# Kernel tuning notes

Measured on AMD Instinct MI355X. Metric: run time of the kernel, lower is better.

Reference implementation:

```python
import jax, jax.numpy as jnp
import numpy as np


def setup_inputs() -> dict:
    key = jax.random.key(0)
    ks = jax.random.split(key, 6)
    T, B, D, H = 512, 64, 512, 512
    s = 1.0 / np.sqrt(H)  # PyTorch-style uniform-ish scale kept simple as scaled normal
    return {
        "inputs": jax.random.normal(ks[0], (T, B, D), jnp.float32),
        "mask": jnp.ones((T, B), jnp.float32),
        "h0": jax.random.normal(ks[1], (B, H), jnp.float32),
        "W_ih": jax.random.normal(ks[2], (4 * H, D), jnp.float32) * s,
        "W_hh": jax.random.normal(ks[3], (4 * H, H), jnp.float32) * s,
        "b_ih": jax.random.normal(ks[4], (4 * H,), jnp.float32) * s,
        "b_hh": jax.random.normal(ks[5], (4 * H,), jnp.float32) * s,
    }


def _lstm_forward(inputs, mask, h0, c0, W_ih, W_hh, b_ih, b_hh):
    """Masked LSTM over time. inputs [T,B,D], mask [T,B], h0/c0 [B,H].
    Mask blend resets state toward the initial hidden where mask==0,
    exactly as the torch loop does per step."""
    bias = b_ih + b_hh
    # Precompute input projections for all steps: [T,B,4H]
    x_proj = jnp.einsum("tbd,gd->tbg", inputs, W_ih) + bias

    def step(carry, inp):
        h, c = carry
        xg, mt = inp  # xg [B,4H], mt [B]
        gates = xg + h @ W_hh.T
        i, f, g, o = jnp.split(gates, 4, axis=-1)
        i = jax.nn.sigmoid(i)
        f = jax.nn.sigmoid(f)
        g = jnp.tanh(g)
        o = jax.nn.sigmoid(o)
        c_new = f * c + i * g
        h_new = o * jnp.tanh(c_new)
        m = mt[:, None]
        h_new = h_new * m + h0 * (1.0 - m)
        c_new = c_new * m + c0 * (1.0 - m)
        return (h_new, c_new), h_new

    (hT, cT), outs = jax.lax.scan(step, (h0, c0), (x_proj, mask))
    return outs, hT, cT


def reference(inputs, mask, h0, W_ih, W_hh, b_ih, b_hh):
    # torch module uses the SAME random tensor for h0 and c0
    out, hT, cT = _lstm_forward(inputs, mask, h0, h0, W_ih, W_hh, b_ih, b_hh)
    # hidden = (stack over layers) -> [1,B,H] each for single layer
    return out, hT[None], cT[None]
```

## Files before the change

### kernel.cpp

```cpp
#include <hip/hip_runtime.h>
#include <hip/hip_fp16.h>


#define T_DIM 512
#define B_DIM 64
#define D_DIM 512
#define H_DIM 512
#define M_DIM (T_DIM * B_DIM)

#define NGROUP 8
#define BPG 32
#define NBLK (NGROUP * BPG)
#define NTHR 512
#define WS 520

typedef __attribute__((ext_vector_type(8))) _Float16 half8;
typedef __attribute__((ext_vector_type(2))) __fp16 fp16x2;
typedef __attribute__((ext_vector_type(4))) float float4v;

#define AT_LD_I(p)    __hip_atomic_load((p), __ATOMIC_RELAXED, __HIP_MEMORY_SCOPE_AGENT)
#define AT_ST_I(p, v) __hip_atomic_store((p), (v), __ATOMIC_RELAXED, __HIP_MEMORY_SCOPE_AGENT)
#define AT_LD64(p)    __hip_atomic_load((p), __ATOMIC_RELAXED, __HIP_MEMORY_SCOPE_AGENT)
#define AT_ST64(p, v) __hip_atomic_store((p), (v), __ATOMIC_RELAXED, __HIP_MEMORY_SCOPE_AGENT)

__device__ __forceinline__ float sigf(float x) { return 1.0f / (1.0f + __expf(-x)); }
__device__ __forceinline__ float tanhfast(float x) { return 2.0f / (1.0f + __expf(-2.0f * x)) - 1.0f; }
__device__ __forceinline__ unsigned short f2h(float x) {
  return __builtin_bit_cast(unsigned short, (_Float16)x);
}
__device__ __forceinline__ unsigned pk2h(float a, float b) {
  fp16x2 h = __builtin_amdgcn_cvt_pkrtz(a, b);
  return __builtin_bit_cast(unsigned, h);
}

__global__ __launch_bounds__(NTHR) void lstm_seq(
    const float* __restrict__ inputs, const float* __restrict__ mask,
    const float* __restrict__ h0, const float* __restrict__ Whh,
    const float* __restrict__ Wih, const float* __restrict__ b_ih,
    const float* __restrict__ b_hh,
    float* __restrict__ out, unsigned short* __restrict__ hbuf,
    int* slot_base) {
  extern __shared__ char smemc[];
  unsigned short* Wl = (unsigned short*)smemc;
  unsigned short* Xw = Wl + 64 * WS;
  unsigned short* hl = Xw + 64 * WS;
  float* part = (float*)(hl + 16 * WS);

  const int tid = threadIdx.x;
  const int blk = blockIdx.x;
  const int grp = blk & 7;
  const int rank = blk >> 3;
  const int bbase = grp * 8;
  const int jbase = rank * 16;
  int* slots = (int*)((char*)slot_base + grp * 128);

  for (int idx = tid; idx < 64 * 128; idx += NTHR) {
    int r = idx >> 7;
    int k4 = (idx & 127) << 2;
    int grow = (r >> 4) * H_DIM + jbase + (r & 15);
    float4 wv = *(const float4*)(Whh + (size_t)grow * H_DIM + k4);
    *(uint2*)(Wl + r * WS + k4) = make_uint2(pk2h(wv.x, wv.y), pk2h(wv.z, wv.w));
    float4 xv = *(const float4*)(Wih + (size_t)grow * D_DIM + k4);
    *(uint2*)(Xw + r * WS + k4) = make_uint2(pk2h(xv.x, xv.y), pk2h(xv.z, xv.w));
  }

  const int eb = tid >> 4, ejl = tid & 15;
  const int bglob = bbase + eb;
  const int jglob = jbase + ejl;
  float h0v = 0.0f, cval = 0.0f, mval = 1.f;
  float bi_ = 0.f, bf_ = 0.f, bg_ = 0.f, bo_ = 0.f;
  if (tid < 128) {
    h0v = h0[bglob * H_DIM + jglob];
    cval = h0v;
    bi_ = b_ih[0 * H_DIM + jglob] + b_hh[0 * H_DIM + jglob];
    bf_ = b_ih[1 * H_DIM + jglob] + b_hh[1 * H_DIM + jglob];
    bg_ = b_ih[2 * H_DIM + jglob] + b_hh[2 * H_DIM + jglob];
    bo_ = b_ih[3 * H_DIM + jglob] + b_hh[3 * H_DIM + jglob];
  }

  {
    int mybits = (tid < 128) ? (int)f2h(h0v) : 0;
    int nb1 = __shfl_down(mybits, 1, 64);
    int nb2 = __shfl_down(mybits, 2, 64);
    int nb3 = __shfl_down(mybits, 3, 64);
    if (tid < 128 && ((ejl & 3) == 0)) {
      unsigned lo = (unsigned)mybits | ((unsigned)nb1 << 16);
      unsigned hi = (unsigned)nb2 | ((unsigned)nb3 << 16);
      AT_ST64((unsigned long long*)hbuf + bglob * 128 + (jglob >> 2),
              ((unsigned long long)hi << 32) | lo);
    }
  }
  __syncthreads();
  if (tid == 0) AT_ST_I(&slots[rank], 1);
  if (tid < 128) mval = mask[bglob];

  const int w = tid >> 6;
  const int lane = tid & 63;
  const int q = w & 3;
  const int ks = w >> 2;
  const int am = lane & 15;
  const int koct = (lane >> 4) * 8;
  const int br = q * 16 + (lane & 15);

  float4v xacc = {0.f, 0.f, 0.f, 0.f};
  {
    const float* xin = inputs + (size_t)bbase * D_DIM;
#pragma unroll
    for (int i = 0; i < 4; ++i) {
      int idx = tid + i * NTHR;
      int r = idx >> 8;
      int cl = idx & 255;
      float2 xv = *(const float2*)(xin + (size_t)r * D_DIM + cl * 2);
      ((unsigned*)hl)[r * (WS / 2) + cl] = pk2h(xv.x, xv.y);
    }
    __syncthreads();
#pragma unroll
    for (int kc = 0; kc < 8; ++kc) {
      int k = ks * 256 + kc * 32 + koct;
      half8 a = *(const half8*)((const _Float16*)hl + am * WS + k);
      half8 b8 = *(const half8*)((const _Float16*)Xw + br * WS + k);
      xacc = __builtin_amdgcn_mfma_f32_16x16x32_f16(a, b8, xacc, 0, 0, 0);
    }
  }
  if (tid < 64) {
    int v;
    do {
      v = (tid < BPG) ? AT_LD_I(&slots[tid]) : 1;
      if (__all(v >= 1)) break;
      __builtin_amdgcn_s_sleep(2);
    } while (true);
  }
  __syncthreads();
  __asm__ volatile("" ::: "memory");

  for (int ts = 0; ts < T_DIM; ++ts) {
    const unsigned long long* cur64 =
        (const unsigned long long*)hbuf + (ts & 1) * (B_DIM * H_DIM / 4) +
        (size_t)bbase * 128;
    unsigned long long* nxt64 =
        (unsigned long long*)hbuf + ((ts + 1) & 1) * (B_DIM * H_DIM / 4);

#pragma unroll
    for (int i = 0; i < 2; ++i) {
      int v = tid + i * NTHR;
      unsigned long long u = AT_LD64(cur64 + v);
      ((unsigned long long*)hl)[(v >> 7) * 130 + (v & 127)] = u;
    }
    __syncthreads();

    float4v acc = xacc;
#pragma unroll
    for (int kc = 0; kc < 8; ++kc) {
      int k = ks * 256 + kc * 32 + koct;
      half8 a = *(const half8*)((const _Float16*)hl + am * WS + k);
      half8 b8 = *(const half8*)((const _Float16*)Wl + br * WS + k);
      acc = __builtin_amdgcn_mfma_f32_16x16x32_f16(a, b8, acc, 0, 0, 0);
    }
#pragma unroll
    for (int reg = 0; reg < 4; ++reg) {
      int m = (lane >> 4) * 4 + reg;
      part[w * 256 + m * 16 + (lane & 15)] = acc[reg];
    }
    __syncthreads();

    float hnew = 0.f;
    if (tid < 128) {
      int o = eb * 16 + ejl;
      float iv = sigf(part[0 * 256 + o] + part[4 * 256 + o] + bi_);
      float fv = sigf(part[1 * 256 + o] + part[5 * 256 + o] + bf_);
      float gv = tanhfast(part[2 * 256 + o] + part[6 * 256 + o] + bg_);
      float ov = sigf(part[3 * 256 + o] + part[7 * 256 + o] + bo_);
      float cn = fv * cval + iv * gv;
      float hn = ov * tanhfast(cn);
      hnew = hn * mval + h0v * (1.0f - mval);
      cval = cn * mval + h0v * (1.0f - mval);
    }
    {
      int mybits = (tid < 128) ? (int)f2h(hnew) : 0;
      int nb1 = __shfl_down(mybits, 1, 64);
      int nb2 = __shfl_down(mybits, 2, 64);
      int nb3 = __shfl_down(mybits, 3, 64);
      if (tid < 128 && ((ejl & 3) == 0)) {
        unsigned lo = (unsigned)mybits | ((unsigned)nb1 << 16);
        unsigned hi = (unsigned)nb2 | ((unsigned)nb3 << 16);
        AT_ST64(nxt64 + bglob * 128 + (jglob >> 2),
                ((unsigned long long)hi << 32) | lo);
      }
    }
    __syncthreads();
    if (tid == 0) AT_ST_I(&slots[rank], ts + 2);

    if (ts + 1 < T_DIM) {
      const float* xin = inputs + ((size_t)(ts + 1) * B_DIM + bbase) * D_DIM;
#pragma unroll
      for (int i = 0; i < 4; ++i) {
        int idx = tid + i * NTHR;
        int r = idx >> 8;
        int cl = idx & 255;
        float2 xv = *(const float2*)(xin + (size_t)r * D_DIM + cl * 2);
        ((unsigned*)hl)[r * (WS / 2) + cl] = pk2h(xv.x, xv.y);
      }
      __syncthreads();
      if (tid < 128) {
        out[((size_t)ts * B_DIM + bglob) * H_DIM + jglob] = hnew;
        mval = mask[(ts + 1) * B_DIM + bglob];
      }
      float4v xa = {0.f, 0.f, 0.f, 0.f};
#pragma unroll
      for (int kc = 0; kc < 8; ++kc) {
        int k = ks * 256 + kc * 32 + koct;
        half8 a = *(const half8*)((const _Float16*)hl + am * WS + k);
        half8 b8 = *(const half8*)((const _Float16*)Xw + br * WS + k);
        xa = __builtin_amdgcn_mfma_f32_16x16x32_f16(a, b8, xa, 0, 0, 0);
      }
      xacc = xa;
    } else if (tid < 128) {
      out[((size_t)ts * B_DIM + bglob) * H_DIM + jglob] = hnew;
      out[(size_t)T_DIM * B_DIM * H_DIM + bglob * H_DIM + jglob] = hnew;
      out[(size_t)T_DIM * B_DIM * H_DIM + B_DIM * H_DIM + bglob * H_DIM + jglob] = cval;
    }

    if (tid < 64) {
      int v;
      do {
        v = (tid < BPG) ? AT_LD_I(&slots[tid]) : (ts + 2);
        if (__all(v >= ts + 2)) break;
        __builtin_amdgcn_s_sleep(2);
      } while (true);
    }
    __syncthreads();
    __asm__ volatile("" ::: "memory");
  }
}

extern "C" void kernel_launch(void* const* d_in, const int* in_sizes, int n_in,
                              void* d_out, int out_size, void* d_ws, size_t ws_size,
                              hipStream_t stream) {
  const float* inputs = (const float*)d_in[0];
  const float* maskp  = (const float*)d_in[1];
  const float* h0     = (const float*)d_in[2];
  const float* W_ih   = (const float*)d_in[3];
  const float* W_hh   = (const float*)d_in[4];
  const float* b_ih   = (const float*)d_in[5];
  const float* b_hh   = (const float*)d_in[6];
  float* out = (float*)d_out;

  char* ws = (char*)d_ws;
  int* slot_base = (int*)ws;
  unsigned short* hbuf = (unsigned short*)(ws + 4096);

  (void)hipMemsetAsync(d_ws, 0, 4096, stream);

  size_t ldsB = (size_t)(64 * WS * 2 * 2 + 16 * WS * 2 + 2048 * 4);

  lstm_seq<<<NBLK, NTHR, ldsB, stream>>>(inputs, maskp, h0, W_hh, W_ih, b_ih, b_hh,
                                         out, hbuf, slot_base);

  (void)in_sizes; (void)n_in; (void)out_size; (void)ws_size;
}
```

Measured before the change: 1.658 ms.

## Interleave two independent batch groups per block to hide cross-block sync latency

Halves the grid to 128 blocks, each owning two batch groups (A and B) that are stepped alternately, so while one group waits on its peer-barrier the other's work can proceed and the spin wait moves to just before consuming h. The input projection is now computed in the same loop as the recurrent MFMA (two accumulators), with next-step inputs prefetched into registers and stored to separate LDS buffers after the step. MFMA A-operand rows are duplicated (am = lane&7) since only 8 batch rows exist, and only half the lanes write partials. This adds serial work per block and doubles per-block step count, trading parallelism for latency hiding.

```diff
diff --git a/kernel.cpp b/kernel.cpp
--- a/kernel.cpp
+++ b/kernel.cpp
@@ -6,11 +6,9 @@
 #define B_DIM 64
 #define D_DIM 512
 #define H_DIM 512
-#define M_DIM (T_DIM * B_DIM)
-
-#define NGROUP 8
+
 #define BPG 32
-#define NBLK (NGROUP * BPG)
+#define NBLK 128
 #define NTHR 512
 #define WS 520
 
@@ -33,6 +31,20 @@
   return __builtin_bit_cast(unsigned, h);
 }
 
+#define SPIN(slots, tgt)                                          \
+  do {                                                            \
+    if (tid < 64) {                                               \
+      int v_;                                                     \
+      do {                                                        \
+        v_ = (tid < BPG) ? AT_LD_I(&(slots)[tid]) : (tgt);        \
+        if (__all(v_ >= (tgt))) break;                            \
+        __builtin_amdgcn_s_sleep(1);                              \
+      } while (true);                                             \
+    }                                                             \
+    __syncthreads();                                              \
+    __asm__ volatile("" ::: "memory");                            \
+  } while (0)
+
 __global__ __launch_bounds__(NTHR) void lstm_seq(
     const float* __restrict__ inputs, const float* __restrict__ mask,
     const float* __restrict__ h0, const float* __restrict__ Whh,
@@ -41,18 +53,22 @@
     float* __restrict__ out, unsigned short* __restrict__ hbuf,
     int* slot_base) {
   extern __shared__ char smemc[];
-  unsigned short* Wl = (unsigned short*)smemc;
-  unsigned short* Xw = Wl + 64 * WS;
-  unsigned short* hl = Xw + 64 * WS;
-  float* part = (float*)(hl + 16 * WS);
+  unsigned short* Wl  = (unsigned short*)smemc;
+  unsigned short* Xw  = Wl + 64 * WS;
+  unsigned short* hl  = Xw + 64 * WS;
+  unsigned short* xsA = hl + 8 * WS;
+  unsigned short* xsB = xsA + 8 * WS;
+  float* part = (float*)(xsB + 8 * WS);
 
   const int tid = threadIdx.x;
   const int blk = blockIdx.x;
-  const int grp = blk & 7;
-  const int rank = blk >> 3;
-  const int bbase = grp * 8;
+  const int gA = blk & 3;
+  const int rank = blk >> 2;
+  const int bbA = gA * 8;
+  const int bbB = bbA + 32;
   const int jbase = rank * 16;
-  int* slots = (int*)((char*)slot_base + grp * 128);
+  int* slotsA = (int*)((char*)slot_base + gA * 128);
+  int* slotsB = (int*)((char*)slot_base + (gA + 4) * 128);
 
   for (int idx = tid; idx < 64 * 128; idx += NTHR) {
     int r = idx >> 7;
@@ -65,171 +81,233 @@
   }
 
   const int eb = tid >> 4, ejl = tid & 15;
-  const int bglob = bbase + eb;
+  const int bglobA = bbA + eb;
+  const int bglobB = bbB + eb;
   const int jglob = jbase + ejl;
-  float h0v = 0.0f, cval = 0.0f, mval = 1.f;
+  float h0vA = 0.f, cvalA = 0.f, mvalA = 1.f;
+  float h0vB = 0.f, cvalB = 0.f, mvalB = 1.f;
   float bi_ = 0.f, bf_ = 0.f, bg_ = 0.f, bo_ = 0.f;
   if (tid < 128) {
-    h0v = h0[bglob * H_DIM + jglob];
-    cval = h0v;
+    h0vA = h0[bglobA * H_DIM + jglob];  cvalA = h0vA;
+    h0vB = h0[bglobB * H_DIM + jglob];  cvalB = h0vB;
     bi_ = b_ih[0 * H_DIM + jglob] + b_hh[0 * H_DIM + jglob];
     bf_ = b_ih[1 * H_DIM + jglob] + b_hh[1 * H_DIM + jglob];
     bg_ = b_ih[2 * H_DIM + jglob] + b_hh[2 * H_DIM + jglob];
     bo_ = b_ih[3 * H_DIM + jglob] + b_hh[3 * H_DIM + jglob];
-  }
+    mvalA = mask[bglobA];
+    mvalB = mask[bglobB];
+  }
+
+  const int xr0r = tid >> 8,           xc = tid & 255;
+  const int xr1r = (tid + 512) >> 8;
+  const int xr2r = (tid + 1024) >> 8;
+  const int xr3r = (tid + 1536) >> 8;
 
   {
-    int mybits = (tid < 128) ? (int)f2h(h0v) : 0;
-    int nb1 = __shfl_down(mybits, 1, 64);
-    int nb2 = __shfl_down(mybits, 2, 64);
-    int nb3 = __shfl_down(mybits, 3, 64);
+    int mbA = (tid < 128) ? (int)f2h(h0vA) : 0;
+    int mbB = (tid < 128) ? (int)f2h(h0vB) : 0;
+    int a1 = __shfl_down(mbA, 1, 64), a2 = __shfl_down(mbA, 2, 64), a3 = __shfl_down(mbA, 3, 64);
+    int b1 = __shfl_down(mbB, 1, 64), b2 = __shfl_down(mbB, 2, 64), b3 = __shfl_down(mbB, 3, 64);
     if (tid < 128 && ((ejl & 3) == 0)) {
-      unsigned lo = (unsigned)mybits | ((unsigned)nb1 << 16);
-      unsigned hi = (unsigned)nb2 | ((unsigned)nb3 << 16);
-      AT_ST64((unsigned long long*)hbuf + bglob * 128 + (jglob >> 2),
-              ((unsigned long long)hi << 32) | lo);
+      unsigned long long uA = ((unsigned long long)(((unsigned)a2) | ((unsigned)a3 << 16)) << 32) |
+                              (((unsigned)mbA) | ((unsigned)a1 << 16));
+      unsigned long long uB = ((unsigned long long)(((unsigned)b2) | ((unsigned)b3 << 16)) << 32) |
+                              (((unsigned)mbB) | ((unsigned)b1 << 16));
+      AT_ST64((unsigned long long*)hbuf + bglobA * 128 + (jglob >> 2), uA);
+      AT_ST64((unsigned long long*)hbuf + bglobB * 128 + (jglob >> 2), uB);
     }
   }
   __syncthreads();
-  if (tid == 0) AT_ST_I(&slots[rank], 1);
-  if (tid < 128) mval = mask[bglob];
+  if (tid == 0) { AT_ST_I(&slotsA[rank], 1); AT_ST_I(&slotsB[rank], 1); }
+
+  {
+    const float* xa = inputs + (size_t)bbA * D_DIM;
+    const float* xb = inputs + (size_t)bbB * D_DIM;
+    float2 t0 = *(const float2*)(xa + (size_t)xr0r * D_DIM + xc * 2);
+    float2 t1 = *(const float2*)(xa + (size_t)xr1r * D_DIM + xc * 2);
+    float2 t2 = *(const float2*)(xa + (size_t)xr2r * D_DIM + xc * 2);
+    float2 t3 = *(const float2*)(xa + (size_t)xr3r * D_DIM + xc * 2);
+    float2 s0 = *(const float2*)(xb + (size_t)xr0r * D_DIM + xc * 2);
+    float2 s1 = *(const float2*)(xb + (size_t)xr1r * D_DIM + xc * 2);
+    float2 s2 = *(const float2*)(xb + (size_t)xr2r * D_DIM + xc * 2);
+    float2 s3 = *(const float2*)(xb + (size_t)xr3r * D_DIM + xc * 2);
+    ((unsigned*)xsA)[xr0r * (WS / 2) + xc] = pk2h(t0.x, t0.y);
+    ((unsigned*)xsA)[xr1r * (WS / 2) + xc] = pk2h(t1.x, t1.y);
+    ((unsigned*)xsA)[xr2r * (WS / 2) + xc] = pk2h(t2.x, t2.y);
+    ((unsigned*)xsA)[xr3r * (WS / 2) + xc] = pk2h(t3.x, t3.y);
+    ((unsigned*)xsB)[xr0r * (WS / 2) + xc] = pk2h(s0.x, s0.y);
+    ((unsigned*)xsB)[xr1r * (WS / 2) + xc] = pk2h(s1.x, s1.y);
+    ((unsigned*)xsB)[xr2r * (WS / 2) + xc] = pk2h(s2.x, s2.y);
+    ((unsigned*)xsB)[xr3r * (WS / 2) + xc] = pk2h(s3.x, s3.y);
+  }
 
   const int w = tid >> 6;
   const int lane = tid & 63;
-  const int q = w & 3;
   const int ks = w >> 2;
-  const int am = lane & 15;
+  const int am = lane & 7;
   const int koct = (lane >> 4) * 8;
-  const int br = q * 16 + (lane & 15);
-
-  float4v xacc = {0.f, 0.f, 0.f, 0.f};
-  {
-    const float* xin = inputs + (size_t)bbase * D_DIM;
-#pragma unroll
-    for (int i = 0; i < 4; ++i) {
-      int idx = tid + i * NTHR;
-      int r = idx >> 8;
-      int cl = idx & 255;
-      float2 xv = *(const float2*)(xin + (size_t)r * D_DIM + cl * 2);
-      ((unsigned*)hl)[r * (WS / 2) + cl] = pk2h(xv.x, xv.y);
-    }
-    __syncthreads();
-#pragma unroll
-    for (int kc = 0; kc < 8; ++kc) {
-      int k = ks * 256 + kc * 32 + koct;
-      half8 a = *(const half8*)((const _Float16*)hl + am * WS + k);
-      half8 b8 = *(const half8*)((const _Float16*)Xw + br * WS + k);
-      xacc = __builtin_amdgcn_mfma_f32_16x16x32_f16(a, b8, xacc, 0, 0, 0);
-    }
-  }
-  if (tid < 64) {
-    int v;
-    do {
-      v = (tid < BPG) ? AT_LD_I(&slots[tid]) : 1;
-      if (__all(v >= 1)) break;
-      __builtin_amdgcn_s_sleep(2);
-    } while (true);
-  }
-  __syncthreads();
-  __asm__ volatile("" ::: "memory");
+  const int br = (w & 3) * 16 + (lane & 15);
 
   for (int ts = 0; ts < T_DIM; ++ts) {
-    const unsigned long long* cur64 =
-        (const unsigned long long*)hbuf + (ts & 1) * (B_DIM * H_DIM / 4) +
-        (size_t)bbase * 128;
-    unsigned long long* nxt64 =
-        (unsigned long long*)hbuf + ((ts + 1) & 1) * (B_DIM * H_DIM / 4);
-
-#pragma unroll
-    for (int i = 0; i < 2; ++i) {
-      int v = tid + i * NTHR;
-      unsigned long long u = AT_LD64(cur64 + v);
-      ((unsigned long long*)hl)[(v >> 7) * 130 + (v & 127)] = u;
-    }
-    __syncthreads();
-
-    float4v acc = xacc;
-#pragma unroll
-    for (int kc = 0; kc < 8; ++kc) {
-      int k = ks * 256 + kc * 32 + koct;
-      half8 a = *(const half8*)((const _Float16*)hl + am * WS + k);
-      half8 b8 = *(const half8*)((const _Float16*)Wl + br * WS + k);
-      acc = __builtin_amdgcn_mfma_f32_16x16x32_f16(a, b8, acc, 0, 0, 0);
-    }
-#pragma unroll
-    for (int reg = 0; reg < 4; ++reg) {
-      int m = (lane >> 4) * 4 + reg;
-      part[w * 256 + m * 16 + (lane & 15)] = acc[reg];
-    }
-    __syncthreads();
-
-    float hnew = 0.f;
-    if (tid < 128) {
-      int o = eb * 16 + ejl;
-      float iv = sigf(part[0 * 256 + o] + part[4 * 256 + o] + bi_);
-      float fv = sigf(part[1 * 256 + o] + part[5 * 256 + o] + bf_);
-      float gv = tanhfast(part[2 * 256 + o] + part[6 * 256 + o] + bg_);
-      float ov = sigf(part[3 * 256 + o] + part[7 * 256 + o] + bo_);
-      float cn = fv * cval + iv * gv;
-      float hn = ov * tanhfast(cn);
-      hnew = hn * mval + h0v * (1.0f - mval);
-      cval = cn * mval + h0v * (1.0f - mval);
-    }
+    const int xts = (ts + 1 < T_DIM) ? ts + 1 : ts;
+
     {
-      int mybits = (tid < 128) ? (int)f2h(hnew) : 0;
-      int nb1 = __shfl_down(mybits, 1, 64);
-      int nb2 = __shfl_down(mybits, 2, 64);
-      int nb3 = __shfl_down(mybits, 3, 64);
-      if (tid < 128 && ((ejl & 3) == 0)) {
-        unsigned lo = (unsigned)mybits | ((unsigned)nb1 << 16);
-        unsigned hi = (unsigned)nb2 | ((unsigned)nb3 << 16);
-        AT_ST64(nxt64 + bglob * 128 + (jglob >> 2),
-                ((unsigned long long)hi << 32) | lo);
-      }
-    }
-    __syncthreads();
-    if (tid == 0) AT_ST_I(&slots[rank], ts + 2);
-
-    if (ts + 1 < T_DIM) {
-      const float* xin = inputs + ((size_t)(ts + 1) * B_DIM + bbase) * D_DIM;
-#pragma unroll
-      for (int i = 0; i < 4; ++i) {
-        int idx = tid + i * NTHR;
-        int r = idx >> 8;
-        int cl = idx & 255;
-        float2 xv = *(const float2*)(xin + (size_t)r * D_DIM + cl * 2);
-        ((unsigned*)hl)[r * (WS / 2) + cl] = pk2h(xv.x, xv.y);
-      }
-      __syncthreads();
-      if (tid < 128) {
-        out[((size_t)ts * B_DIM + bglob) * H_DIM + jglob] = hnew;
-        mval = mask[(ts + 1) * B_DIM + bglob];
-      }
-      float4v xa = {0.f, 0.f, 0.f, 0.f};
+      const unsigned long long* cur =
+          (const unsigned long long*)hbuf + (ts & 1) * (B_DIM * H_DIM / 4) + (size_t)bbA * 128;
+      unsigned long long* nxt =
+          (unsigned long long*)hbuf + ((ts + 1) & 1) * (B_DIM * H_DIM / 4);
+
+      SPIN(slotsA, ts + 1);
+
+      unsigned long long hld0 = AT_LD64(cur + tid);
+      unsigned long long hld1 = AT_LD64(cur + tid + NTHR);
+      const float* xin = inputs + ((size_t)xts * B_DIM + bbA) * D_DIM;
+      float2 a0 = *(const float2*)(xin + (size_t)xr0r * D_DIM + xc * 2);
+      float2 a1 = *(const float2*)(xin + (size_t)xr1r * D_DIM + xc * 2);
+      float2 a2 = *(const float2*)(xin + (size_t)xr2r * D_DIM + xc * 2);
+      float2 a3 = *(const float2*)(xin + (size_t)xr3r * D_DIM + xc * 2);
+      ((unsigned long long*)hl)[(tid >> 7) * 130 + (tid & 127)] = hld0;
+      { int v2 = tid + NTHR; ((unsigned long long*)hl)[(v2 >> 7) * 130 + (v2 & 127)] = hld1; }
+      __syncthreads();
+
+      float4v aH = {0.f, 0.f, 0.f, 0.f}, aX = {0.f, 0.f, 0.f, 0.f};
 #pragma unroll
       for (int kc = 0; kc < 8; ++kc) {
         int k = ks * 256 + kc * 32 + koct;
-        half8 a = *(const half8*)((const _Float16*)hl + am * WS + k);
-        half8 b8 = *(const half8*)((const _Float16*)Xw + br * WS + k);
-        xa = __builtin_amdgcn_mfma_f32_16x16x32_f16(a, b8, xa, 0, 0, 0);
-      }
-      xacc = xa;
-    } else if (tid < 128) {
-      out[((size_t)ts * B_DIM + bglob) * H_DIM + jglob] = hnew;
-      out[(size_t)T_DIM * B_DIM * H_DIM + bglob * H_DIM + jglob] = hnew;
-      out[(size_t)T_DIM * B_DIM * H_DIM + B_DIM * H_DIM + bglob * H_DIM + jglob] = cval;
+        half8 ah = *(const half8*)((const _Float16*)hl + am * WS + k);
+        half8 bh = *(const half8*)((const _Float16*)Wl + br * WS + k);
+        aH = __builtin_amdgcn_mfma_f32_16x16x32_f16(ah, bh, aH, 0, 0, 0);
+        half8 ax = *(const half8*)((const _Float16*)xsA + am * WS + k);
+        half8 bx = *(const half8*)((const _Float16*)Xw + br * WS + k);
+        aX = __builtin_amdgcn_mfma_f32_16x16x32_f16(ax, bx, aX, 0, 0, 0);
+      }
+      float4v acc = aH + aX;
+      if (lane < 32) {
+#pragma unroll
+        for (int reg = 0; reg < 4; ++reg) {
+          int m = (lane >> 4) * 4 + reg;
+          part[w * 128 + m * 16 + (lane & 15)] = acc[reg];
+        }
+      }
+      __syncthreads();
+
+      float hnew = 0.f;
+      if (tid < 128) {
+        int o = eb * 16 + ejl;
+        float iv = sigf(part[0 * 128 + o] + part[4 * 128 + o] + bi_);
+        float fv = sigf(part[1 * 128 + o] + part[5 * 128 + o] + bf_);
+        float gv = tanhfast(part[2 * 128 + o] + part[6 * 128 + o] + bg_);
+        float ov = sigf(part[3 * 128 + o] + part[7 * 128 + o] + bo_);
+        float cn = fv * cvalA + iv * gv;
+        float hn = ov * tanhfast(cn);
+        hnew = hn * mvalA + h0vA * (1.f - mvalA);
+        cvalA = cn * mvalA + h0vA * (1.f - mvalA);
+      }
+      {
+        int mb = (tid < 128) ? (int)f2h(hnew) : 0;
+        int n1 = __shfl_down(mb, 1, 64), n2 = __shfl_down(mb, 2, 64), n3 = __shfl_down(mb, 3, 64);
+        if (tid < 128 && ((ejl & 3) == 0)) {
+          unsigned long long u = ((unsigned long long)(((unsigned)n2) | ((unsigned)n3 << 16)) << 32) |
+                                 (((unsigned)mb) | ((unsigned)n1 << 16));
+          AT_ST64(nxt + bglobA * 128 + (jglob >> 2), u);
+        }
+      }
+      __syncthreads();
+      if (tid == 0) AT_ST_I(&slotsA[rank], ts + 2);
+
+      ((unsigned*)xsA)[xr0r * (WS / 2) + xc] = pk2h(a0.x, a0.y);
+      ((unsigned*)xsA)[xr1r * (WS / 2) + xc] = pk2h(a1.x, a1.y);
+      ((unsigned*)xsA)[xr2r * (WS / 2) + xc] = pk2h(a2.x, a2.y);
+      ((unsigned*)xsA)[xr3r * (WS / 2) + xc] = pk2h(a3.x, a3.y);
+      if (tid < 128) {
+        out[((size_t)ts * B_DIM + bglobA) * H_DIM + jglob] = hnew;
+        if (ts == T_DIM - 1) {
+          out[(size_t)T_DIM * B_DIM * H_DIM + bglobA * H_DIM + jglob] = hnew;
+          out[(size_t)T_DIM * B_DIM * H_DIM + B_DIM * H_DIM + bglobA * H_DIM + jglob] = cvalA;
+        } else {
+          mvalA = mask[(ts + 1) * B_DIM + bglobA];
+        }
+      }
     }
 
-    if (tid < 64) {
-      int v;
-      do {
-        v = (tid < BPG) ? AT_LD_I(&slots[tid]) : (ts + 2);
-        if (__all(v >= ts + 2)) break;
-        __builtin_amdgcn_s_sleep(2);
-      } while (true);
+    {
+      const unsigned long long* cur =
+          (const unsigned long long*)hbuf + (ts & 1) * (B_DIM * H_DIM / 4) + (size_t)bbB * 128;
+      unsigned long long* nxt =
+          (unsigned long long*)hbuf + ((ts + 1) & 1) * (B_DIM * H_DIM / 4);
+
+      SPIN(slotsB, ts + 1);
+
+      unsigned long long hld0 = AT_LD64(cur + tid);
+      unsigned long long hld1 = AT_LD64(cur + tid + NTHR);
+      const float* xin = inputs + ((size_t)xts * B_DIM + bbB) * D_DIM;
+      float2 a0 = *(const float2*)(xin + (size_t)xr0r * D_DIM + xc * 2);
+      float2 a1 = *(const float2*)(xin + (size_t)xr1r * D_DIM + xc * 2);
+      float2 a2 = *(const float2*)(xin + (size_t)xr2r * D_DIM + xc * 2);
+      float2 a3 = *(const float2*)(xin + (size_t)xr3r * D_DIM + xc * 2);
+      ((unsigned long long*)hl)[(tid >> 7) * 130 + (tid & 127)] = hld0;
+      { int v2 = tid + NTHR; ((unsigned long long*)hl)[(v2 >> 7) * 130 + (v2 & 127)] = hld1; }
+      __syncthreads();
+
+      float4v aH = {0.f, 0.f, 0.f, 0.f}, aX = {0.f, 0.f, 0.f, 0.f};
+#pragma unroll
+      for (int kc = 0; kc < 8; ++kc) {
+        int k = ks * 256 + kc * 32 + koct;
+        half8 ah = *(const half8*)((const _Float16*)hl + am * WS + k);
+        half8 bh = *(const half8*)((const _Float16*)Wl + br * WS + k);
+        aH = __builtin_amdgcn_mfma_f32_16x16x32_f16(ah, bh, aH, 0, 0, 0);
+        half8 ax = *(const half8*)((const _Float16*)xsB + am * WS + k);
+        half8 bx = *(const half8*)((const _Float16*)Xw + br * WS + k);
+        aX = __builtin_amdgcn_mfma_f32_16x16x32_f16(ax, bx, aX, 0, 0, 0);
+      }
+      float4v acc = aH + aX;
+      if (lane < 32) {
+#pragma unroll
+        for (int reg = 0; reg < 4; ++reg) {
+          int m = (lane >> 4) * 4 + reg;
+          part[w * 128 + m * 16 + (lane & 15)] = acc[reg];
+        }
+      }
+      __syncthreads();
+
+      float hnew = 0.f;
+      if (tid < 128) {
+        int o = eb * 16 + ejl;
+        float iv = sigf(part[0 * 128 + o] + part[4 * 128 + o] + bi_);
+        float fv = sigf(part[1 * 128 + o] + part[5 * 128 + o] + bf_);
+        float gv = tanhfast(part[2 * 128 + o] + part[6 * 128 + o] + bg_);
+        float ov = sigf(part[3 * 128 + o] + part[7 * 128 + o] + bo_);
+        float cn = fv * cvalB + iv * gv;
+        float hn = ov * tanhfast(cn);
+        hnew = hn * mvalB + h0vB * (1.f - mvalB);
+        cvalB = cn * mvalB + h0vB * (1.f - mvalB);
+      }
+      {
+        int mb = (tid < 128) ? (int)f2h(hnew) : 0;
+        int n1 = __shfl_down(mb, 1, 64), n2 = __shfl_down(mb, 2, 64), n3 = __shfl_down(mb, 3, 64);
+        if (tid < 128 && ((ejl & 3) == 0)) {
+          unsigned long long u = ((unsigned long long)(((unsigned)n2) | ((unsigned)n3 << 16)) << 32) |
+                                 (((unsigned)mb) | ((unsigned)n1 << 16));
+          AT_ST64(nxt + bglobB * 128 + (jglob >> 2), u);
+        }
+      }
+      __syncthreads();
+      if (tid == 0) AT_ST_I(&slotsB[rank], ts + 2);
+
+      ((unsigned*)xsB)[xr0r * (WS / 2) + xc] = pk2h(a0.x, a0.y);
+      ((unsigned*)xsB)[xr1r * (WS / 2) + xc] = pk2h(a1.x, a1.y);
+      ((unsigned*)xsB)[xr2r * (WS / 2) + xc] = pk2h(a2.x, a2.y);
+      ((unsigned*)xsB)[xr3r * (WS / 2) + xc] = pk2h(a3.x, a3.y);
+      if (tid < 128) {
+        out[((size_t)ts * B_DIM + bglobB) * H_DIM + jglob] = hnew;
+        if (ts == T_DIM - 1) {
+          out[(size_t)T_DIM * B_DIM * H_DIM + bglobB * H_DIM + jglob] = hnew;
+          out[(size_t)T_DIM * B_DIM * H_DIM + B_DIM * H_DIM + bglobB * H_DIM + jglob] = cvalB;
+        } else {
+          mvalB = mask[(ts + 1) * B_DIM + bglobB];
+        }
+      }
     }
-    __syncthreads();
-    __asm__ volatile("" ::: "memory");
   }
 }
 
@@ -251,7 +329,7 @@
 
   (void)hipMemsetAsync(d_ws, 0, 4096, stream);
 
-  size_t ldsB = (size_t)(64 * WS * 2 * 2 + 16 * WS * 2 + 2048 * 4);
+  size_t ldsB = (size_t)(64 * WS * 2 * 2 + 3 * 8 * WS * 2 + 8 * 128 * 4);
 
   lstm_seq<<<NBLK, NTHR, ldsB, stream>>>(inputs, maskp, h0, W_hh, W_ih, b_ih, b_hh,
                                          out, hbuf, slot_base);
```

New measurement: 2.733 ms. +64.8%, slower.
